# Kernel tuning notes

Measured on AMD Instinct MI355X. Metric: run time of the kernel, lower is better.

The kernel has to match this reference:

```python
import jax, jax.numpy as jnp
import numpy as np

B, NF, NU = 8, 64, 1024
DF, DU, DH, H = 64, 32, 128, 8


def setup_inputs() -> dict:
    key = jax.random.key(0)
    ks = jax.random.split(key, 10)
    s = 0.05  # keep logits in a stable range
    return {
        "f0": jax.random.normal(ks[0], (B, NF, DF), jnp.float32),
        "u0": jax.random.normal(ks[1], (B, NU, DU), jnp.float32),
        "f1": jax.random.normal(ks[2], (B, NF, DF), jnp.float32),
        "u1": jax.random.normal(ks[3], (B, NU, DU), jnp.float32),
        "Wf": jax.random.normal(ks[4], (H, 2, 3, DF, DH), jnp.float32) * s,
        "bf": jax.random.normal(ks[5], (H, 2, 3, DH), jnp.float32) * s,
        "Wu": jax.random.normal(ks[6], (H, 2, 3, DU, DH), jnp.float32) * s,
        "bu": jax.random.normal(ks[7], (H, 2, 3, DH), jnp.float32) * s,
        "Wout": jax.random.normal(ks[8], (H * DH, DH), jnp.float32) * s,
        "bout": jax.random.normal(ks[9], (DH,), jnp.float32) * s,
    }


def _proj(x, W, b):
    # x: [B,N,Din], W: [H,3,Din,DH], b: [H,3,DH] -> [3,B,H,N,DH] (qkv-major)
    y = jnp.einsum('bnf,hkfd->kbhnd', x, W)
    return y + b.transpose(1, 0, 2)[:, None, :, None, :]


def reference(f0, u0, f1, u1, Wf, bf, Wu, bu, Wout, bout):
    # per-head per-player Q/K/V projections; concat order: [f0, u0, f1, u1]
    parts = [
        _proj(f0, Wf[:, 0], bf[:, 0]),
        _proj(u0, Wu[:, 0], bu[:, 0]),
        _proj(f1, Wf[:, 1], bf[:, 1]),
        _proj(u1, Wu[:, 1], bu[:, 1]),
    ]
    qkv = jnp.concatenate(parts, axis=3)  # [3,B,H,S,DH]
    Q, K, V = qkv[0], qkv[1], qkv[2]
    scale = jnp.asarray(DH ** 0.5, Q.dtype)
    scores = jnp.einsum('bhqd,bhkd->bhqk', Q, K) / scale  # [B,H,S,S]
    attn = jax.nn.softmax(scores, axis=-1)
    out = jnp.einsum('bhqk,bhkd->bhqd', attn, V)  # [B,H,S,DH]
    # concat heads along feature dim (head order preserved), then final linear
    S = out.shape[2]
    out = out.transpose(0, 2, 1, 3).reshape(out.shape[0], S, H * DH)
    return out @ Wout + bout  # [B,S,DH]
```

## Files before the change

kernel.cpp:

```cpp
#include <hip/hip_runtime.h>
#include <hip/hip_bf16.h>

#define BB 8
#define NFQ 64
#define NUQ 1024
#define HH 8
#define SS 2176

typedef __attribute__((ext_vector_type(8))) short short8;
typedef __attribute__((ext_vector_type(4))) float f32x4;
typedef __attribute__((ext_vector_type(2))) unsigned int uint2_t;
typedef unsigned short ubf;

__device__ __forceinline__ ubf f2bf(float x) {
    unsigned u = __float_as_uint(x);
    u = u + 0x7fffu + ((u >> 16) & 1u);
    return (ubf)(u >> 16);
}
__device__ __forceinline__ unsigned pkbf(float a, float b) {
    __hip_bfloat162 h = __float22bfloat162_rn(make_float2(a, b));
    union { __hip_bfloat162 hh; unsigned u; } c; c.hh = h;
    return c.u;
}
__device__ __forceinline__ float bf2f(short v) {
    return __uint_as_float(((unsigned)(ubf)v) << 16);
}

__global__ __launch_bounds__(256) void prep_kernel(
    const float* __restrict__ Wf, const float* __restrict__ Wu, const float* __restrict__ Wout,
    ubf* __restrict__ WfT, ubf* __restrict__ WuT, ubf* __restrict__ WoutT)
{
    __shared__ ubf tl[128 * 72];
    const int idx = blockIdx.x, tid = threadIdx.x;
    const float* src; ubf* dst; int F, dstride;
    if (idx < 48)       { F = 64; src = Wf + (size_t)idx * 64 * 128;        dst = WfT + (size_t)idx * 128 * 64;        dstride = 64; }
    else if (idx < 96)  { F = 32; src = Wu + (size_t)(idx - 48) * 32 * 128; dst = WuT + (size_t)(idx - 48) * 128 * 32; dstride = 32; }
    else                { F = 64; int s = idx - 96; src = Wout + (size_t)s * 64 * 128; dst = WoutT + s * 64; dstride = 1024; }
    const int pitch = F + 8;
    for (int i = tid; i < F * 32; i += 256) {
        int f = i >> 5, d0 = (i & 31) * 4;
        f32x4 v = *(const f32x4*)&src[f * 128 + d0];
        tl[(d0 + 0) * pitch + f] = f2bf(v[0]);
        tl[(d0 + 1) * pitch + f] = f2bf(v[1]);
        tl[(d0 + 2) * pitch + f] = f2bf(v[2]);
        tl[(d0 + 3) * pitch + f] = f2bf(v[3]);
    }
    __syncthreads();
    if (F == 64) {
        int d = tid >> 1, half = tid & 1;
#pragma unroll
        for (int jj = 0; jj < 4; ++jj)
            *(short8*)&dst[(size_t)d * dstride + half * 32 + jj * 8] =
                *(const short8*)&tl[d * pitch + half * 32 + jj * 8];
    } else {
        int d = tid & 127, fh = tid >> 7;
#pragma unroll
        for (int jj = 0; jj < 2; ++jj)
            *(short8*)&dst[(size_t)d * dstride + fh * 16 + jj * 8] =
                *(const short8*)&tl[d * pitch + fh * 16 + jj * 8];
    }
}

__global__ __launch_bounds__(256) void proj_kernel(
    const float* __restrict__ f0, const float* __restrict__ u0,
    const float* __restrict__ f1, const float* __restrict__ u1,
    const ubf* __restrict__ WfT, const ubf* __restrict__ WuT,
    const float* __restrict__ bfv, const float* __restrict__ buv,
    ubf* __restrict__ Qg, ubf* __restrict__ Kg, ubf* __restrict__ Vtg)
{
    __shared__ ubf xlds[32 * 64];
    __shared__ ubf outq[32 * 136];
    __shared__ ubf outk[32 * 136];
    __shared__ ubf outv[128 * 40];

    const int tid = threadIdx.x;
    const int bh = blockIdx.x / 17, j = blockIdx.x % 17;
    const int b = bh >> 3, h = bh & 7;
    const int w = tid >> 6, l = tid & 63, lg = l >> 4, dl = l & 15;
    const int dg0 = w * 2;

    const bool isF = (j == 0);
    const f32x4 zf = {0.f, 0.f, 0.f, 0.f};

    short8 af[3][2][2];
    f32x4 bv[3][2];

    const int up = isF ? 0 : ((j - 1) >> 3);
    const int ugrp = isF ? 0 : ((j - 1) & 7);
    const float* xpb = 0;
    if (!isF) xpb = (up ? u1 : u0) + (size_t)b * NUQ * 32;

    for (int c4 = 0; c4 < 4; ++c4) {
        int p, n0, s0;
        const float* xp;
        if (isF) {
            p = c4 >> 1; n0 = (c4 & 1) * 32;
            s0 = p ? 1088 + (c4 & 1) * 32 : (c4 & 1) * 32;
            xp = (p ? f1 : f0) + (size_t)b * NFQ * 64;
        } else {
            p = up; int c = ugrp * 4 + c4; n0 = 32 * c;
            s0 = (p ? 1152 : 64) + 32 * c;
            xp = xpb;
        }

        if (c4 == 0 || (isF && c4 == 2)) {
            if (isF) {
                const ubf* wt = WfT + (size_t)((h * 2 + p) * 3) * 8192;
#pragma unroll
                for (int k = 0; k < 3; ++k)
#pragma unroll
                    for (int g = 0; g < 2; ++g) {
                        af[k][g][0] = *(const short8*)&wt[(size_t)k * 8192 + ((dg0 + g) * 16 + dl) * 64 + lg * 8];
                        af[k][g][1] = *(const short8*)&wt[(size_t)k * 8192 + ((dg0 + g) * 16 + dl) * 64 + 32 + lg * 8];
                        bv[k][g] = *(const f32x4*)&bfv[((h * 2 + p) * 3 + k) * 128 + (dg0 + g) * 16 + 4 * lg];
                    }
            } else {
                const ubf* wt = WuT + (size_t)((h * 2 + p) * 3) * 4096;
#pragma unroll
                for (int k = 0; k < 3; ++k)
#pragma unroll
                    for (int g = 0; g < 2; ++g) {
                        af[k][g][0] = *(const short8*)&wt[(size_t)k * 4096 + ((dg0 + g) * 16 + dl) * 32 + lg * 8];
                        bv[k][g] = *(const f32x4*)&buv[((h * 2 + p) * 3 + k) * 128 + (dg0 + g) * 16 + 4 * lg];
                    }
            }
        }

        if (isF) {
            int row = tid >> 3, g = tid & 7;
            const float* s = &xp[(size_t)(n0 + row) * 64 + g * 8];
            f32x4 v0 = *(const f32x4*)&s[0];
            f32x4 v1 = *(const f32x4*)&s[4];
            union { unsigned u[4]; short8 s8; } pk;
            pk.u[0] = pkbf(v0[0], v0[1]); pk.u[1] = pkbf(v0[2], v0[3]);
            pk.u[2] = pkbf(v1[0], v1[1]); pk.u[3] = pkbf(v1[2], v1[3]);
            *(short8*)&xlds[row * 64 + ((g ^ (row & 7)) * 8)] = pk.s8;
        } else if (tid < 128) {
            int row = tid >> 2, g = tid & 3;
            const float* s = &xp[(size_t)(n0 + row) * 32 + g * 8];
            f32x4 v0 = *(const f32x4*)&s[0];
            f32x4 v1 = *(const f32x4*)&s[4];
            union { unsigned u[4]; short8 s8; } pk;
            pk.u[0] = pkbf(v0[0], v0[1]); pk.u[1] = pkbf(v0[2], v0[3]);
            pk.u[2] = pkbf(v1[0], v1[1]); pk.u[3] = pkbf(v1[2], v1[3]);
            *(short8*)&xlds[row * 64 + ((g ^ (row & 7)) * 8)] = pk.s8;
        }
        __syncthreads();

        short8 bx0[2], bx1[2];
#pragma unroll
        for (int tile = 0; tile < 2; ++tile) {
            const int row = tile * 16 + dl;
            bx0[tile] = *(const short8*)&xlds[row * 64 + ((lg ^ (row & 7)) * 8)];
            if (isF)
                bx1[tile] = *(const short8*)&xlds[row * 64 + (((4 + lg) ^ (row & 7)) * 8)];
        }

#pragma unroll
        for (int k = 0; k < 3; ++k)
#pragma unroll
            for (int g = 0; g < 2; ++g)
#pragma unroll
                for (int tile = 0; tile < 2; ++tile) {
                    f32x4 acc = __builtin_amdgcn_mfma_f32_16x16x32_bf16(af[k][g][0], bx0[tile], zf, 0, 0, 0);
                    if (isF)
                        acc = __builtin_amdgcn_mfma_f32_16x16x32_bf16(af[k][g][1], bx1[tile], acc, 0, 0, 0);
                    if (k < 2) {
                        ubf* o = k ? outk : outq;
                        uint2_t wv;
                        wv.x = pkbf(acc[0] + bv[k][g][0], acc[1] + bv[k][g][1]);
                        wv.y = pkbf(acc[2] + bv[k][g][2], acc[3] + bv[k][g][3]);
                        *(uint2_t*)&o[(tile * 16 + dl) * 136 + (dg0 + g) * 16 + 4 * lg] = wv;
                    } else {
                        int pos = (dl & 3) + 8 * ((dl >> 2) & 3) + 4 * tile;
#pragma unroll
                        for (int r = 0; r < 4; ++r)
                            outv[((dg0 + g) * 16 + 4 * lg + r) * 40 + pos] = f2bf(acc[r] + bv[2][g][r]);
                    }
                }
        __syncthreads();

        {
            int row = tid >> 3, c16 = (tid & 7) * 16;
            size_t qbase = ((size_t)bh * SS + s0 + row) * 128 + c16;
            *(short8*)&Qg[qbase]     = *(const short8*)&outq[row * 136 + c16];
            *(short8*)&Qg[qbase + 8] = *(const short8*)&outq[row * 136 + c16 + 8];
            *(short8*)&Kg[qbase]     = *(const short8*)&outk[row * 136 + c16];
            *(short8*)&Kg[qbase + 8] = *(const short8*)&outk[row * 136 + c16 + 8];
            int dd = tid >> 1, half = tid & 1;
            size_t vbase = ((size_t)bh * 128 + dd) * SS + s0 + half * 16;
            *(short8*)&Vtg[vbase]     = *(const short8*)&outv[dd * 40 + half * 16];
            *(short8*)&Vtg[vbase + 8] = *(const short8*)&outv[dd * 40 + half * 16 + 8];
        }
    }
}

__global__ __launch_bounds__(512) void attn_kernel(
    const ubf* __restrict__ Qg, const ubf* __restrict__ Kg, const ubf* __restrict__ Vtg,
    ubf* __restrict__ attnout)
{
    __shared__ ubf Klds[2][32 * 128];
    __shared__ ubf Vlds[2][128 * 40];

    const int tid = threadIdx.x;
    const int swz = (blockIdx.x & 7) * 72 + (blockIdx.x >> 3);
    const int bh = swz / 9;
    const int qc = swz % 9;
    const int b = bh >> 3, h = bh & 7;
    const int w = tid >> 6, l = tid & 63, lg = l >> 4, dl = l & 15;
    int qbase = qc * 256 + w * 32;
    const bool qvalid = qbase < SS;
    if (!qvalid) qbase = SS - 32;
    const int qr0 = qbase + dl;

    const ubf* Qbh = Qg + (size_t)bh * SS * 128;
    const ubf* Kbh = Kg + (size_t)bh * SS * 128;
    const ubf* Vbh = Vtg + (size_t)bh * 128 * SS;

    short8 qfa[4], qfb[4];
#pragma unroll
    for (int dc = 0; dc < 4; ++dc) {
        qfa[dc] = *(const short8*)&Qbh[(size_t)qr0 * 128 + dc * 32 + lg * 8];
        qfb[dc] = *(const short8*)&Qbh[(size_t)(qr0 + 16) * 128 + dc * 32 + lg * 8];
    }

    f32x4 otA[8], otB[8];
    const f32x4 zf = {0.f, 0.f, 0.f, 0.f};
#pragma unroll
    for (int i = 0; i < 8; ++i) { otA[i] = zf; otB[i] = zf; }
    float lsA = 0.f, lsB = 0.f;

    const int skrow = tid >> 4, skc = tid & 15;
    const int svrow = tid >> 2, svc = tid & 3;
    const float sc = 0.08838834764831845f * 1.44269504088896340736f;

    short8 kst, vst;
    const ubf* kp = &Kbh[(size_t)skrow * 128 + skc * 8];
    const ubf* vp = &Vbh[(size_t)svrow * SS + svc * 8];
    const int ko = skrow * 128 + ((skc * 8) ^ ((skrow & 7) << 3));
    const int vo = svrow * 40 + svc * 8;

    kst = *(const short8*)&kp[0];
    vst = *(const short8*)&vp[0];
    *(short8*)&Klds[0][ko] = kst;
    *(short8*)&Vlds[0][vo] = vst;
    __syncthreads();

    int cur = 0;
    for (int it = 0; it < 68; ++it) {
        if (it < 67) {
            const int nb = (it + 1) * 32;
            kst = *(const short8*)&kp[(size_t)nb * 128];
            vst = *(const short8*)&vp[nb];
        }
        const ubf* Kc = Klds[cur];
        const ubf* Vc = Vlds[cur];

        f32x4 s0a = zf, s1a = zf, s0b = zf, s1b = zf;
        __builtin_amdgcn_s_setprio(1);
#pragma unroll
        for (int dc = 0; dc < 4; ++dc) {
            const int col = (dc * 32 + lg * 8) ^ ((dl & 7) << 3);
            short8 k0 = *(const short8*)&Kc[dl * 128 + col];
            short8 k1 = *(const short8*)&Kc[(16 + dl) * 128 + col];
            s0a = __builtin_amdgcn_mfma_f32_16x16x32_bf16(k0, qfa[dc], s0a, 0, 0, 0);
            s1a = __builtin_amdgcn_mfma_f32_16x16x32_bf16(k1, qfa[dc], s1a, 0, 0, 0);
            s0b = __builtin_amdgcn_mfma_f32_16x16x32_bf16(k0, qfb[dc], s0b, 0, 0, 0);
            s1b = __builtin_amdgcn_mfma_f32_16x16x32_bf16(k1, qfb[dc], s1b, 0, 0, 0);
        }
        __builtin_amdgcn_s_setprio(0);

        float pa[8], pb[8];
#pragma unroll
        for (int r = 0; r < 4; ++r) {
            pa[r]     = __builtin_amdgcn_exp2f(s0a[r] * sc);
            pa[4 + r] = __builtin_amdgcn_exp2f(s1a[r] * sc);
            pb[r]     = __builtin_amdgcn_exp2f(s0b[r] * sc);
            pb[4 + r] = __builtin_amdgcn_exp2f(s1b[r] * sc);
        }
        lsA += ((pa[0]+pa[1]) + (pa[2]+pa[3])) + ((pa[4]+pa[5]) + (pa[6]+pa[7]));
        lsB += ((pb[0]+pb[1]) + (pb[2]+pb[3])) + ((pb[4]+pb[5]) + (pb[6]+pb[7]));

        union { unsigned u[4]; short8 s; } Pa, Pb;
        Pa.u[0] = pkbf(pa[0], pa[1]); Pa.u[1] = pkbf(pa[2], pa[3]);
        Pa.u[2] = pkbf(pa[4], pa[5]); Pa.u[3] = pkbf(pa[6], pa[7]);
        Pb.u[0] = pkbf(pb[0], pb[1]); Pb.u[1] = pkbf(pb[2], pb[3]);
        Pb.u[2] = pkbf(pb[4], pb[5]); Pb.u[3] = pkbf(pb[6], pb[7]);

        __builtin_amdgcn_s_setprio(1);
#pragma unroll
        for (int dt = 0; dt < 8; ++dt) {
            short8 vf = *(const short8*)&Vc[(dt * 16 + dl) * 40 + lg * 8];
            otA[dt] = __builtin_amdgcn_mfma_f32_16x16x32_bf16(vf, Pa.s, otA[dt], 0, 0, 0);
            otB[dt] = __builtin_amdgcn_mfma_f32_16x16x32_bf16(vf, Pb.s, otB[dt], 0, 0, 0);
        }
        __builtin_amdgcn_s_setprio(0);

        if (it < 67) {
            ubf* Kn = Klds[cur ^ 1];
            ubf* Vn = Vlds[cur ^ 1];
            *(short8*)&Kn[ko] = kst;
            *(short8*)&Vn[vo] = vst;
            cur ^= 1;
            __syncthreads();
        }
    }

    if (qvalid) {
        lsA += __shfl_xor(lsA, 16); lsA += __shfl_xor(lsA, 32);
        lsB += __shfl_xor(lsB, 16); lsB += __shfl_xor(lsB, 32);
        const float invA = 1.f / lsA, invB = 1.f / lsB;

        ubf* dstA = attnout + ((size_t)b * SS + qr0) * 1024 + h * 128;
        ubf* dstB = attnout + ((size_t)b * SS + qr0 + 16) * 1024 + h * 128;
#pragma unroll
        for (int dt = 0; dt < 8; ++dt) {
            f32x4 oA = otA[dt] * invA;
            f32x4 oB = otB[dt] * invB;
            uint2_t wA, wB;
            wA.x = pkbf(oA[0], oA[1]); wA.y = pkbf(oA[2], oA[3]);
            wB.x = pkbf(oB[0], oB[1]); wB.y = pkbf(oB[2], oB[3]);
            *(uint2_t*)&dstA[dt * 16 + 4 * lg] = wA;
            *(uint2_t*)&dstB[dt * 16 + 4 * lg] = wB;
        }
    }
}

__global__ __launch_bounds__(256) void outproj_kernel(
    const ubf* __restrict__ attnout, const ubf* __restrict__ WoutT,
    const float* __restrict__ bout, float* __restrict__ out)
{
    __shared__ ubf alds[32 * 1024];
    const int tid = threadIdx.x;
    const int row0 = blockIdx.x * 32;
    const int w = tid >> 6, l = tid & 63, lg = l >> 4, dl = l & 15;
    const int dg0 = w * 2;
    const f32x4 zf = {0.f, 0.f, 0.f, 0.f};

#pragma unroll
    for (int pz = 0; pz < 2; ++pz) {
        int row = pz * 16 + (tid >> 4);
        int cl = tid & 15;
#pragma unroll
        for (int jj = 0; jj < 8; ++jj) {
            int g = cl + 16 * jj;
            short8 v = *(const short8*)&attnout[(size_t)(row0 + row) * 1024 + g * 8];
            *(short8*)&alds[row * 1024 + ((g ^ (row & 7)) * 8)] = v;
        }
    }
    __syncthreads();

    f32x4 acc[2][2];
    acc[0][0] = zf; acc[0][1] = zf; acc[1][0] = zf; acc[1][1] = zf;

    for (int dc = 0; dc < 32; ++dc) {
        short8 a0 = *(const short8*)&WoutT[(size_t)((dg0 + 0) * 16 + dl) * 1024 + dc * 32 + lg * 8];
        short8 a1 = *(const short8*)&WoutT[(size_t)((dg0 + 1) * 16 + dl) * 1024 + dc * 32 + lg * 8];
        short8 b0 = *(const short8*)&alds[dl * 1024 + (((dc * 4 + lg) ^ (dl & 7)) * 8)];
        short8 b1 = *(const short8*)&alds[(16 + dl) * 1024 + (((dc * 4 + lg) ^ (dl & 7)) * 8)];
        acc[0][0] = __builtin_amdgcn_mfma_f32_16x16x32_bf16(a0, b0, acc[0][0], 0, 0, 0);
        acc[0][1] = __builtin_amdgcn_mfma_f32_16x16x32_bf16(a0, b1, acc[0][1], 0, 0, 0);
        acc[1][0] = __builtin_amdgcn_mfma_f32_16x16x32_bf16(a1, b0, acc[1][0], 0, 0, 0);
        acc[1][1] = __builtin_amdgcn_mfma_f32_16x16x32_bf16(a1, b1, acc[1][1], 0, 0, 0);
    }

#pragma unroll
    for (int g = 0; g < 2; ++g) {
        f32x4 bb = *(const f32x4*)&bout[(dg0 + g) * 16 + 4 * lg];
#pragma unroll
        for (int tile = 0; tile < 2; ++tile) {
            f32x4 o = acc[g][tile] + bb;
            *(f32x4*)&out[((size_t)row0 + tile * 16 + dl) * 128 + (dg0 + g) * 16 + 4 * lg] = o;
        }
    }
}

extern "C" void kernel_launch(void* const* d_in, const int* in_sizes, int n_in,
                              void* d_out, int out_size, void* d_ws, size_t ws_size,
                              hipStream_t stream) {
    const float* f0  = (const float*)d_in[0];
    const float* u0  = (const float*)d_in[1];
    const float* f1  = (const float*)d_in[2];
    const float* u1  = (const float*)d_in[3];
    const float* Wf  = (const float*)d_in[4];
    const float* bfv = (const float*)d_in[5];
    const float* Wu  = (const float*)d_in[6];
    const float* buv = (const float*)d_in[7];
    const float* Wout = (const float*)d_in[8];
    const float* bout = (const float*)d_in[9];
    float* out = (float*)d_out;

    char* ws = (char*)d_ws;
    const size_t qkv_bytes = (size_t)BB * HH * SS * 128 * sizeof(ubf);
    ubf* Qg  = (ubf*)ws;
    ubf* Kg  = (ubf*)(ws + qkv_bytes);
    ubf* Vtg = (ubf*)(ws + 2 * qkv_bytes);
    ubf* attnout = (ubf*)(ws + 3 * qkv_bytes);
    ubf* WfT   = (ubf*)(ws + 4 * qkv_bytes);
    ubf* WuT   = (ubf*)(ws + 4 * qkv_bytes + 786432);
    ubf* WoutT = (ubf*)(ws + 4 * qkv_bytes + 786432 + 393216);

    prep_kernel<<<dim3(112), dim3(256), 0, stream>>>(Wf, Wu, Wout, WfT, WuT, WoutT);
    proj_kernel<<<dim3(64 * 17), dim3(256), 0, stream>>>(f0, u0, f1, u1, WfT, WuT, bfv, buv, Qg, Kg, Vtg);
    attn_kernel<<<dim3(576), dim3(512), 0, stream>>>(Qg, Kg, Vtg, attnout);
    outproj_kernel<<<dim3(544), dim3(256), 0, stream>>>(attnout, WoutT, bout, out);
}
```

Before: 290.9 us.

## Double the attention key tile to 64 and XOR-swizzle the V LDS layout

```diff
diff --git a/kernel.cpp b/kernel.cpp
--- a/kernel.cpp
+++ b/kernel.cpp
@@ -199,8 +199,8 @@
     const ubf* __restrict__ Qg, const ubf* __restrict__ Kg, const ubf* __restrict__ Vtg,
     ubf* __restrict__ attnout)
 {
-    __shared__ ubf Klds[2][32 * 128];
-    __shared__ ubf Vlds[2][128 * 40];
+    __shared__ ubf Klds[2][64 * 128];
+    __shared__ ubf Vlds[2][128 * 64];
 
     const int tid = threadIdx.x;
     const int swz = (blockIdx.x & 7) * 72 + (blockIdx.x >> 3);
@@ -230,77 +230,103 @@
     for (int i = 0; i < 8; ++i) { otA[i] = zf; otB[i] = zf; }
     float lsA = 0.f, lsB = 0.f;
 
-    const int skrow = tid >> 4, skc = tid & 15;
+    const int skrow = tid >> 3, skc = tid & 7;
     const int svrow = tid >> 2, svc = tid & 3;
     const float sc = 0.08838834764831845f * 1.44269504088896340736f;
 
-    short8 kst, vst;
-    const ubf* kp = &Kbh[(size_t)skrow * 128 + skc * 8];
-    const ubf* vp = &Vbh[(size_t)svrow * SS + svc * 8];
-    const int ko = skrow * 128 + ((skc * 8) ^ ((skrow & 7) << 3));
-    const int vo = svrow * 40 + svc * 8;
-
-    kst = *(const short8*)&kp[0];
-    vst = *(const short8*)&vp[0];
-    *(short8*)&Klds[0][ko] = kst;
-    *(short8*)&Vlds[0][vo] = vst;
+    const int ksw = (skrow & 7) << 3;
+    const int ko0 = skrow * 128 + ((skc * 16) ^ ksw);
+    const int ko1 = skrow * 128 + ((skc * 16 + 8) ^ ksw);
+    const int vr7 = svrow & 7;
+    const int vo0 = svrow * 64 + (((2 * svc)     ^ vr7) * 8);
+    const int vo1 = svrow * 64 + (((2 * svc + 1) ^ vr7) * 8);
+    const ubf* kp = &Kbh[(size_t)skrow * 128 + skc * 16];
+    const ubf* vp = &Vbh[(size_t)svrow * SS + svc * 16];
+    const int pvs = (dl & 7) << 3;
+
+    short8 k0s, k1s, v0s, v1s;
+    k0s = *(const short8*)&kp[0];
+    k1s = *(const short8*)&kp[8];
+    v0s = *(const short8*)&vp[0];
+    v1s = *(const short8*)&vp[8];
+    *(short8*)&Klds[0][ko0] = k0s;
+    *(short8*)&Klds[0][ko1] = k1s;
+    *(short8*)&Vlds[0][vo0] = v0s;
+    *(short8*)&Vlds[0][vo1] = v1s;
     __syncthreads();
 
     int cur = 0;
-    for (int it = 0; it < 68; ++it) {
-        if (it < 67) {
-            const int nb = (it + 1) * 32;
-            kst = *(const short8*)&kp[(size_t)nb * 128];
-            vst = *(const short8*)&vp[nb];
+    for (int it = 0; it < 34; ++it) {
+        if (it < 33) {
+            const size_t nb = (size_t)(it + 1) * 64;
+            k0s = *(const short8*)&kp[nb * 128];
+            k1s = *(const short8*)&kp[nb * 128 + 8];
+            v0s = *(const short8*)&vp[nb];
+            v1s = *(const short8*)&vp[nb + 8];
         }
         const ubf* Kc = Klds[cur];
         const ubf* Vc = Vlds[cur];
 
         f32x4 s0a = zf, s1a = zf, s0b = zf, s1b = zf;
+        f32x4 t0a = zf, t1a = zf, t0b = zf, t1b = zf;
         __builtin_amdgcn_s_setprio(1);
 #pragma unroll
         for (int dc = 0; dc < 4; ++dc) {
-            const int col = (dc * 32 + lg * 8) ^ ((dl & 7) << 3);
+            const int col = (dc * 32 + lg * 8) ^ pvs;
             short8 k0 = *(const short8*)&Kc[dl * 128 + col];
             short8 k1 = *(const short8*)&Kc[(16 + dl) * 128 + col];
+            short8 k2 = *(const short8*)&Kc[(32 + dl) * 128 + col];
+            short8 k3 = *(const short8*)&Kc[(48 + dl) * 128 + col];
             s0a = __builtin_amdgcn_mfma_f32_16x16x32_bf16(k0, qfa[dc], s0a, 0, 0, 0);
             s1a = __builtin_amdgcn_mfma_f32_16x16x32_bf16(k1, qfa[dc], s1a, 0, 0, 0);
+            t0a = __builtin_amdgcn_mfma_f32_16x16x32_bf16(k2, qfa[dc], t0a, 0, 0, 0);
+            t1a = __builtin_amdgcn_mfma_f32_16x16x32_bf16(k3, qfa[dc], t1a, 0, 0, 0);
             s0b = __builtin_amdgcn_mfma_f32_16x16x32_bf16(k0, qfb[dc], s0b, 0, 0, 0);
             s1b = __builtin_amdgcn_mfma_f32_16x16x32_bf16(k1, qfb[dc], s1b, 0, 0, 0);
+            t0b = __builtin_amdgcn_mfma_f32_16x16x32_bf16(k2, qfb[dc], t0b, 0, 0, 0);
+            t1b = __builtin_amdgcn_mfma_f32_16x16x32_bf16(k3, qfb[dc], t1b, 0, 0, 0);
         }
         __builtin_amdgcn_s_setprio(0);
 
-        float pa[8], pb[8];
-#pragma unroll
-        for (int r = 0; r < 4; ++r) {
-            pa[r]     = __builtin_amdgcn_exp2f(s0a[r] * sc);
-            pa[4 + r] = __builtin_amdgcn_exp2f(s1a[r] * sc);
-            pb[r]     = __builtin_amdgcn_exp2f(s0b[r] * sc);
-            pb[4 + r] = __builtin_amdgcn_exp2f(s1b[r] * sc);
-        }
-        lsA += ((pa[0]+pa[1]) + (pa[2]+pa[3])) + ((pa[4]+pa[5]) + (pa[6]+pa[7]));
-        lsB += ((pb[0]+pb[1]) + (pb[2]+pb[3])) + ((pb[4]+pb[5]) + (pb[6]+pb[7]));
-
-        union { unsigned u[4]; short8 s; } Pa, Pb;
-        Pa.u[0] = pkbf(pa[0], pa[1]); Pa.u[1] = pkbf(pa[2], pa[3]);
-        Pa.u[2] = pkbf(pa[4], pa[5]); Pa.u[3] = pkbf(pa[6], pa[7]);
-        Pb.u[0] = pkbf(pb[0], pb[1]); Pb.u[1] = pkbf(pb[2], pb[3]);
-        Pb.u[2] = pkbf(pb[4], pb[5]); Pb.u[3] = pkbf(pb[6], pb[7]);
+        union { unsigned u[4]; short8 s; } Pa0, Pa1, Pb0, Pb1;
+#define EXPPACK(lo, hi, P, lsum) { \
+            float e0 = __builtin_amdgcn_exp2f(lo[0] * sc); \
+            float e1 = __builtin_amdgcn_exp2f(lo[1] * sc); \
+            float e2 = __builtin_amdgcn_exp2f(lo[2] * sc); \
+            float e3 = __builtin_amdgcn_exp2f(lo[3] * sc); \
+            float e4 = __builtin_amdgcn_exp2f(hi[0] * sc); \
+            float e5 = __builtin_amdgcn_exp2f(hi[1] * sc); \
+            float e6 = __builtin_amdgcn_exp2f(hi[2] * sc); \
+            float e7 = __builtin_amdgcn_exp2f(hi[3] * sc); \
+            lsum += ((e0 + e1) + (e2 + e3)) + ((e4 + e5) + (e6 + e7)); \
+            P.u[0] = pkbf(e0, e1); P.u[1] = pkbf(e2, e3); \
+            P.u[2] = pkbf(e4, e5); P.u[3] = pkbf(e6, e7); }
+        EXPPACK(s0a, s1a, Pa0, lsA);
+        EXPPACK(t0a, t1a, Pa1, lsA);
+        EXPPACK(s0b, s1b, Pb0, lsB);
+        EXPPACK(t0b, t1b, Pb1, lsB);
+#undef EXPPACK
 
         __builtin_amdgcn_s_setprio(1);
 #pragma unroll
         for (int dt = 0; dt < 8; ++dt) {
-            short8 vf = *(const short8*)&Vc[(dt * 16 + dl) * 40 + lg * 8];
-            otA[dt] = __builtin_amdgcn_mfma_f32_16x16x32_bf16(vf, Pa.s, otA[dt], 0, 0, 0);
-            otB[dt] = __builtin_amdgcn_mfma_f32_16x16x32_bf16(vf, Pb.s, otB[dt], 0, 0, 0);
+            const int vrow = (dt * 16 + dl) * 64;
+            short8 vf0 = *(const short8*)&Vc[vrow + ((lg * 8) ^ pvs)];
+            short8 vf1 = *(const short8*)&Vc[vrow + (((4 + lg) * 8) ^ pvs)];
+            otA[dt] = __builtin_amdgcn_mfma_f32_16x16x32_bf16(vf0, Pa0.s, otA[dt], 0, 0, 0);
+            otA[dt] = __builtin_amdgcn_mfma_f32_16x16x32_bf16(vf1, Pa1.s, otA[dt], 0, 0, 0);
+            otB[dt] = __builtin_amdgcn_mfma_f32_16x16x32_bf16(vf0, Pb0.s, otB[dt], 0, 0, 0);
+            otB[dt] = __builtin_amdgcn_mfma_f32_16x16x32_bf16(vf1, Pb1.s, otB[dt], 0, 0, 0);
         }
         __builtin_amdgcn_s_setprio(0);
 
-        if (it < 67) {
+        if (it < 33) {
             ubf* Kn = Klds[cur ^ 1];
             ubf* Vn = Vlds[cur ^ 1];
-            *(short8*)&Kn[ko] = kst;
-            *(short8*)&Vn[vo] = vst;
+            *(short8*)&Kn[ko0] = k0s;
+            *(short8*)&Kn[ko1] = k1s;
+            *(short8*)&Vn[vo0] = v0s;
+            *(short8*)&Vn[vo1] = v1s;
             cur ^= 1;
             __syncthreads();
         }
```

New measurement: 275.4 us. -5.3%, faster.

## Retile attention: 48 queries per wave, 64-key tiles, swizzled V LDS

Applied to the files above, without the earlier changes.

```diff
diff --git a/kernel.cpp b/kernel.cpp
--- a/kernel.cpp
+++ b/kernel.cpp
@@ -195,133 +195,159 @@
     }
 }
 
-__global__ __launch_bounds__(512) void attn_kernel(
+__global__ __launch_bounds__(256) void attn_kernel(
     const ubf* __restrict__ Qg, const ubf* __restrict__ Kg, const ubf* __restrict__ Vtg,
     ubf* __restrict__ attnout)
 {
-    __shared__ ubf Klds[2][32 * 128];
-    __shared__ ubf Vlds[2][128 * 40];
+    __shared__ ubf Klds[2][64 * 128];
+    __shared__ ubf Vlds[2][128 * 64];
 
     const int tid = threadIdx.x;
-    const int swz = (blockIdx.x & 7) * 72 + (blockIdx.x >> 3);
-    const int bh = swz / 9;
-    const int qc = swz % 9;
+    const int swz = (blockIdx.x & 7) * 96 + (blockIdx.x >> 3);
+    const int bh = swz / 12;
+    const int qc = swz % 12;
     const int b = bh >> 3, h = bh & 7;
     const int w = tid >> 6, l = tid & 63, lg = l >> 4, dl = l & 15;
-    int qbase = qc * 256 + w * 32;
-    const bool qvalid = qbase < SS;
-    if (!qvalid) qbase = SS - 32;
-    const int qr0 = qbase + dl;
+    const int qbase = qc * 192 + w * 48;
 
     const ubf* Qbh = Qg + (size_t)bh * SS * 128;
     const ubf* Kbh = Kg + (size_t)bh * SS * 128;
     const ubf* Vbh = Vtg + (size_t)bh * 128 * SS;
 
-    short8 qfa[4], qfb[4];
-#pragma unroll
-    for (int dc = 0; dc < 4; ++dc) {
-        qfa[dc] = *(const short8*)&Qbh[(size_t)qr0 * 128 + dc * 32 + lg * 8];
-        qfb[dc] = *(const short8*)&Qbh[(size_t)(qr0 + 16) * 128 + dc * 32 + lg * 8];
-    }
-
-    f32x4 otA[8], otB[8];
+    int qs[3]; bool qv[3];
+#pragma unroll
+    for (int s = 0; s < 3; ++s) {
+        int q0 = qbase + s * 16;
+        qv[s] = q0 < SS;
+        qs[s] = (qv[s] ? q0 : SS - 16) + dl;
+    }
+
+    short8 qf[3][4];
+#pragma unroll
+    for (int s = 0; s < 3; ++s)
+#pragma unroll
+        for (int dc = 0; dc < 4; ++dc)
+            qf[s][dc] = *(const short8*)&Qbh[(size_t)qs[s] * 128 + dc * 32 + lg * 8];
+
+    f32x4 ot[3][8];
     const f32x4 zf = {0.f, 0.f, 0.f, 0.f};
 #pragma unroll
-    for (int i = 0; i < 8; ++i) { otA[i] = zf; otB[i] = zf; }
-    float lsA = 0.f, lsB = 0.f;
-
-    const int skrow = tid >> 4, skc = tid & 15;
-    const int svrow = tid >> 2, svc = tid & 3;
+    for (int s = 0; s < 3; ++s)
+#pragma unroll
+        for (int i = 0; i < 8; ++i) ot[s][i] = zf;
+    float lsum[3] = {0.f, 0.f, 0.f};
+
     const float sc = 0.08838834764831845f * 1.44269504088896340736f;
 
-    short8 kst, vst;
-    const ubf* kp = &Kbh[(size_t)skrow * 128 + skc * 8];
-    const ubf* vp = &Vbh[(size_t)svrow * SS + svc * 8];
-    const int ko = skrow * 128 + ((skc * 8) ^ ((skrow & 7) << 3));
-    const int vo = svrow * 40 + svc * 8;
-
-    kst = *(const short8*)&kp[0];
-    vst = *(const short8*)&vp[0];
-    *(short8*)&Klds[0][ko] = kst;
-    *(short8*)&Vlds[0][vo] = vst;
+    const int lh = l >> 4;
+    const int ldsw = w * 2048 + l * 8;
+    const int kr0 = w * 16 + lh;
+    const int vd0 = w * 32 + (l >> 3);
+    const int vgc = ((l & 7) ^ ((l >> 3) & 7)) * 8;
+
+    short8 ks[4], vs[4];
+#pragma unroll
+    for (int j = 0; j < 4; ++j) {
+        int r = kr0 + j * 4;
+        int g = ((l & 15) ^ (r & 7)) * 8;
+        ks[j] = *(const short8*)&Kbh[(size_t)r * 128 + g];
+        vs[j] = *(const short8*)&Vbh[(size_t)(vd0 + j * 8) * SS + vgc];
+    }
+#pragma unroll
+    for (int j = 0; j < 4; ++j) {
+        *(short8*)&Klds[0][ldsw + j * 512] = ks[j];
+        *(short8*)&Vlds[0][ldsw + j * 512] = vs[j];
+    }
     __syncthreads();
 
     int cur = 0;
-    for (int it = 0; it < 68; ++it) {
-        if (it < 67) {
-            const int nb = (it + 1) * 32;
-            kst = *(const short8*)&kp[(size_t)nb * 128];
-            vst = *(const short8*)&vp[nb];
+    for (int it = 0; it < 34; ++it) {
+        if (it < 33) {
+            const size_t kb = (size_t)(it + 1) * 64;
+#pragma unroll
+            for (int j = 0; j < 4; ++j) {
+                int r = kr0 + j * 4;
+                int g = ((l & 15) ^ (r & 7)) * 8;
+                ks[j] = *(const short8*)&Kbh[(kb + r) * 128 + g];
+                vs[j] = *(const short8*)&Vbh[(size_t)(vd0 + j * 8) * SS + kb + vgc];
+            }
         }
         const ubf* Kc = Klds[cur];
         const ubf* Vc = Vlds[cur];
 
-        f32x4 s0a = zf, s1a = zf, s0b = zf, s1b = zf;
-        __builtin_amdgcn_s_setprio(1);
-#pragma unroll
-        for (int dc = 0; dc < 4; ++dc) {
-            const int col = (dc * 32 + lg * 8) ^ ((dl & 7) << 3);
-            short8 k0 = *(const short8*)&Kc[dl * 128 + col];
-            short8 k1 = *(const short8*)&Kc[(16 + dl) * 128 + col];
-            s0a = __builtin_amdgcn_mfma_f32_16x16x32_bf16(k0, qfa[dc], s0a, 0, 0, 0);
-            s1a = __builtin_amdgcn_mfma_f32_16x16x32_bf16(k1, qfa[dc], s1a, 0, 0, 0);
-            s0b = __builtin_amdgcn_mfma_f32_16x16x32_bf16(k0, qfb[dc], s0b, 0, 0, 0);
-            s1b = __builtin_amdgcn_mfma_f32_16x16x32_bf16(k1, qfb[dc], s1b, 0, 0, 0);
-        }
-        __builtin_amdgcn_s_setprio(0);
-
-        float pa[8], pb[8];
-#pragma unroll
-        for (int r = 0; r < 4; ++r) {
-            pa[r]     = __builtin_amdgcn_exp2f(s0a[r] * sc);
-            pa[4 + r] = __builtin_amdgcn_exp2f(s1a[r] * sc);
-            pb[r]     = __builtin_amdgcn_exp2f(s0b[r] * sc);
-            pb[4 + r] = __builtin_amdgcn_exp2f(s1b[r] * sc);
-        }
-        lsA += ((pa[0]+pa[1]) + (pa[2]+pa[3])) + ((pa[4]+pa[5]) + (pa[6]+pa[7]));
-        lsB += ((pb[0]+pb[1]) + (pb[2]+pb[3])) + ((pb[4]+pb[5]) + (pb[6]+pb[7]));
-
-        union { unsigned u[4]; short8 s; } Pa, Pb;
-        Pa.u[0] = pkbf(pa[0], pa[1]); Pa.u[1] = pkbf(pa[2], pa[3]);
-        Pa.u[2] = pkbf(pa[4], pa[5]); Pa.u[3] = pkbf(pa[6], pa[7]);
-        Pb.u[0] = pkbf(pb[0], pb[1]); Pb.u[1] = pkbf(pb[2], pb[3]);
-        Pb.u[2] = pkbf(pb[4], pb[5]); Pb.u[3] = pkbf(pb[6], pb[7]);
-
-        __builtin_amdgcn_s_setprio(1);
-#pragma unroll
-        for (int dt = 0; dt < 8; ++dt) {
-            short8 vf = *(const short8*)&Vc[(dt * 16 + dl) * 40 + lg * 8];
-            otA[dt] = __builtin_amdgcn_mfma_f32_16x16x32_bf16(vf, Pa.s, otA[dt], 0, 0, 0);
-            otB[dt] = __builtin_amdgcn_mfma_f32_16x16x32_bf16(vf, Pb.s, otB[dt], 0, 0, 0);
-        }
-        __builtin_amdgcn_s_setprio(0);
-
-        if (it < 67) {
-            ubf* Kn = Klds[cur ^ 1];
-            ubf* Vn = Vlds[cur ^ 1];
-            *(short8*)&Kn[ko] = kst;
-            *(short8*)&Vn[vo] = vst;
+#pragma unroll
+        for (int kh = 0; kh < 2; ++kh) {
+            f32x4 s0[3], s1[3];
+#pragma unroll
+            for (int s = 0; s < 3; ++s) { s0[s] = zf; s1[s] = zf; }
+
+            __builtin_amdgcn_s_setprio(1);
+#pragma unroll
+            for (int dc = 0; dc < 4; ++dc) {
+                const int col = ((dc * 4 + lg) ^ (dl & 7)) * 8;
+                short8 k0 = *(const short8*)&Kc[(kh * 32 + dl) * 128 + col];
+                short8 k1 = *(const short8*)&Kc[(kh * 32 + 16 + dl) * 128 + col];
+#pragma unroll
+                for (int s = 0; s < 3; ++s) {
+                    s0[s] = __builtin_amdgcn_mfma_f32_16x16x32_bf16(k0, qf[s][dc], s0[s], 0, 0, 0);
+                    s1[s] = __builtin_amdgcn_mfma_f32_16x16x32_bf16(k1, qf[s][dc], s1[s], 0, 0, 0);
+                }
+            }
+            __builtin_amdgcn_s_setprio(0);
+
+            union { unsigned u[4]; short8 s8; } P[3];
+#pragma unroll
+            for (int s = 0; s < 3; ++s) {
+                float e0 = __builtin_amdgcn_exp2f(s0[s][0] * sc);
+                float e1 = __builtin_amdgcn_exp2f(s0[s][1] * sc);
+                float e2 = __builtin_amdgcn_exp2f(s0[s][2] * sc);
+                float e3 = __builtin_amdgcn_exp2f(s0[s][3] * sc);
+                float e4 = __builtin_amdgcn_exp2f(s1[s][0] * sc);
+                float e5 = __builtin_amdgcn_exp2f(s1[s][1] * sc);
+                float e6 = __builtin_amdgcn_exp2f(s1[s][2] * sc);
+                float e7 = __builtin_amdgcn_exp2f(s1[s][3] * sc);
+                lsum[s] += ((e0 + e1) + (e2 + e3)) + ((e4 + e5) + (e6 + e7));
+                P[s].u[0] = pkbf(e0, e1); P[s].u[1] = pkbf(e2, e3);
+                P[s].u[2] = pkbf(e4, e5); P[s].u[3] = pkbf(e6, e7);
+            }
+
+            __builtin_amdgcn_s_setprio(1);
+#pragma unroll
+            for (int dt = 0; dt < 8; ++dt) {
+                short8 vf = *(const short8*)&Vc[(dt * 16 + dl) * 64 + (((kh * 4 + lg) ^ (dl & 7)) * 8)];
+#pragma unroll
+                for (int s = 0; s < 3; ++s)
+                    ot[s][dt] = __builtin_amdgcn_mfma_f32_16x16x32_bf16(vf, P[s].s8, ot[s][dt], 0, 0, 0);
+            }
+            __builtin_amdgcn_s_setprio(0);
+        }
+
+        if (it < 33) {
+#pragma unroll
+            for (int j = 0; j < 4; ++j) {
+                *(short8*)&Klds[cur ^ 1][ldsw + j * 512] = ks[j];
+                *(short8*)&Vlds[cur ^ 1][ldsw + j * 512] = vs[j];
+            }
             cur ^= 1;
             __syncthreads();
         }
     }
 
-    if (qvalid) {
-        lsA += __shfl_xor(lsA, 16); lsA += __shfl_xor(lsA, 32);
-        lsB += __shfl_xor(lsB, 16); lsB += __shfl_xor(lsB, 32);
-        const float invA = 1.f / lsA, invB = 1.f / lsB;
-
-        ubf* dstA = attnout + ((size_t)b * SS + qr0) * 1024 + h * 128;
-        ubf* dstB = attnout + ((size_t)b * SS + qr0 + 16) * 1024 + h * 128;
-#pragma unroll
-        for (int dt = 0; dt < 8; ++dt) {
-            f32x4 oA = otA[dt] * invA;
-            f32x4 oB = otB[dt] * invB;
-            uint2_t wA, wB;
-            wA.x = pkbf(oA[0], oA[1]); wA.y = pkbf(oA[2], oA[3]);
-            wB.x = pkbf(oB[0], oB[1]); wB.y = pkbf(oB[2], oB[3]);
-            *(uint2_t*)&dstA[dt * 16 + 4 * lg] = wA;
-            *(uint2_t*)&dstB[dt * 16 + 4 * lg] = wB;
+#pragma unroll
+    for (int s = 0; s < 3; ++s) {
+        float ls = lsum[s];
+        ls += __shfl_xor(ls, 16);
+        ls += __shfl_xor(ls, 32);
+        const float inv = 1.f / ls;
+        if (qv[s]) {
+            ubf* dst = attnout + ((size_t)b * SS + qs[s]) * 1024 + h * 128;
+#pragma unroll
+            for (int dt = 0; dt < 8; ++dt) {
+                f32x4 o = ot[s][dt] * inv;
+                uint2_t wv;
+                wv.x = pkbf(o[0], o[1]); wv.y = pkbf(o[2], o[3]);
+                *(uint2_t*)&dst[dt * 16 + 4 * lg] = wv;
+            }
         }
     }
 }
@@ -402,6 +428,6 @@
 
     prep_kernel<<<dim3(112), dim3(256), 0, stream>>>(Wf, Wu, Wout, WfT, WuT, WoutT);
     proj_kernel<<<dim3(64 * 17), dim3(256), 0, stream>>>(f0, u0, f1, u1, WfT, WuT, bfv, buv, Qg, Kg, Vtg);
-    attn_kernel<<<dim3(576), dim3(512), 0, stream>>>(Qg, Kg, Vtg, attnout);
+    attn_kernel<<<dim3(768), dim3(256), 0, stream>>>(Qg, Kg, Vtg, attnout);
     outproj_kernel<<<dim3(544), dim3(256), 0, stream>>>(attnout, WoutT, bout, out);
 }
```

Result: slower. 304.6 us (+4.7%).
